# Performance work log

Hardware: AMD Instinct MI355X
Metric: run time of the kernel (lower is better)

## Reference

```python
import jax, jax.numpy as jnp
import numpy as np

N_NODES = 131072
N_EDGES = 1048576
N_FEAT = 8
H = 128
H6 = 256
N_PROB = 64


def _gru_cell(m, h, Wih, Whh, bih, bhh):
    # PyTorch GRUCell semantics
    gi = m @ Wih.T + bih  # [N, 3H]
    gh = h @ Whh.T + bhh
    i_r, i_z, i_n = jnp.split(gi, 3, axis=-1)
    h_r, h_z, h_n = jnp.split(gh, 3, axis=-1)
    r = jax.nn.sigmoid(i_r + h_r)
    z = jax.nn.sigmoid(i_z + h_z)
    n = jnp.tanh(i_n + r * h_n)
    return (1.0 - z) * n + z * h


def _gated_graph_conv(x, src, dst, ew, W, Wih, Whh, bih, bhh):
    # PyG GatedGraphConv(out_channels=H, num_layers=2); in_channels == out_channels so no padding
    h = x
    for l in range(2):
        t = h @ W[l]                      # node-level transform [N, H]
        msg = t[src] * ew[:, None]        # gather + edge scaling [E, H]
        agg = jax.ops.segment_sum(msg, dst, num_segments=x.shape[0])  # scatter-add
        h = _gru_cell(agg, h, Wih, Whh, bih, bhh)
    return h


def _forward(G, edge_index, edge_weight, edge_attribute, segment_ids,
             W_emb1, b_emb1, W_emb2, b_emb2,
             conv1_W, conv1_Wih, conv1_Whh, conv1_bih, conv1_bhh,
             conv2_W, conv2_Wih, conv2_Whh, conv2_bih, conv2_bhh,
             W_g1, b_g1, W_g2, b_g2, W_l, b_l, W_l2, b_l2, W_l3, b_l3):
    src, dst = edge_index[0], edge_index[1]
    x = jax.nn.relu(G @ W_emb1 + b_emb1)
    x = jax.nn.relu(x @ W_emb2 + b_emb2)
    x = jax.nn.relu(_gated_graph_conv(x, src, dst, edge_weight, conv1_W, conv1_Wih, conv1_Whh, conv1_bih, conv1_bhh))
    x = jax.nn.relu(_gated_graph_conv(x, src, dst, edge_weight, conv2_W, conv2_Wih, conv2_Whh, conv2_bih, conv2_bhh))
    x = jax.nn.relu(x @ W_g1 + b_g1)
    x = x @ W_g2 + b_g2                   # node embeddings [N, H]
    # per-problem segment mean (replaces the python loop over contiguous slices)
    sums = jax.ops.segment_sum(x, segment_ids, num_segments=N_PROB)
    counts = jax.ops.segment_sum(jnp.ones((x.shape[0], 1), x.dtype), segment_ids, num_segments=N_PROB)
    gmean = sums / jnp.maximum(counts, 1.0)
    u = jnp.concatenate([x, gmean[segment_ids]], axis=-1)  # [N, 2H]
    u = jax.nn.relu(u @ W_l + b_l)
    u = jax.nn.relu(u @ W_l2 + b_l2)
    u = u @ W_l3 + b_l3                   # [N, 1]
    return u


def setup_inputs() -> dict:
    key = jax.random.key(0)
    ks = jax.random.split(key, 40)
    s = 0.05
    rn = lambda k, shp: (jax.random.normal(k, shp, jnp.float32) * s)
    inp = {}
    inp["G"] = jax.random.normal(ks[0], (N_NODES, N_FEAT), jnp.float32)
    inp["edge_index"] = jax.random.randint(ks[1], (2, N_EDGES), 0, N_NODES, jnp.int32)
    inp["edge_weight"] = jax.random.uniform(ks[2], (N_EDGES,), jnp.float32)
    inp["edge_attribute"] = jax.random.normal(ks[3], (N_EDGES,), jnp.float32)
    inp["segment_ids"] = jnp.sort(jax.random.randint(ks[4], (N_NODES,), 0, N_PROB, jnp.int32))
    inp["W_emb1"] = rn(ks[5], (N_FEAT, H)); inp["b_emb1"] = jnp.zeros((H,), jnp.float32)
    inp["W_emb2"] = rn(ks[6], (H, H));      inp["b_emb2"] = jnp.zeros((H,), jnp.float32)
    inp["conv1_W"] = rn(ks[7], (2, H, H))
    inp["conv1_Wih"] = rn(ks[8], (3 * H, H)); inp["conv1_Whh"] = rn(ks[9], (3 * H, H))
    inp["conv1_bih"] = jnp.zeros((3 * H,), jnp.float32); inp["conv1_bhh"] = jnp.zeros((3 * H,), jnp.float32)
    inp["conv2_W"] = rn(ks[10], (2, H, H))
    inp["conv2_Wih"] = rn(ks[11], (3 * H, H)); inp["conv2_Whh"] = rn(ks[12], (3 * H, H))
    inp["conv2_bih"] = jnp.zeros((3 * H,), jnp.float32); inp["conv2_bhh"] = jnp.zeros((3 * H,), jnp.float32)
    inp["W_g1"] = rn(ks[13], (H, H)); inp["b_g1"] = jnp.zeros((H,), jnp.float32)
    inp["W_g2"] = rn(ks[14], (H, H)); inp["b_g2"] = jnp.zeros((H,), jnp.float32)
    inp["W_l"] = rn(ks[15], (2 * H, H6)); inp["b_l"] = jnp.zeros((H6,), jnp.float32)
    inp["W_l2"] = rn(ks[16], (H6, H)); inp["b_l2"] = jnp.zeros((H,), jnp.float32)
    inp["W_l3"] = rn(ks[17], (H, 1)); inp["b_l3"] = jnp.zeros((1,), jnp.float32)
    return inp


def reference(G, edge_index, edge_weight, edge_attribute, segment_ids,
              W_emb1, b_emb1, W_emb2, b_emb2,
              conv1_W, conv1_Wih, conv1_Whh, conv1_bih, conv1_bhh,
              conv2_W, conv2_Wih, conv2_Whh, conv2_bih, conv2_bhh,
              W_g1, b_g1, W_g2, b_g2, W_l, b_l, W_l2, b_l2, W_l3, b_l3):
    return _forward(G, edge_index, edge_weight, edge_attribute, segment_ids,
                    W_emb1, b_emb1, W_emb2, b_emb2,
                    conv1_W, conv1_Wih, conv1_Whh, conv1_bih, conv1_bhh,
                    conv2_W, conv2_Wih, conv2_Whh, conv2_bih, conv2_bhh,
                    W_g1, b_g1, W_g2, b_g2, W_l, b_l, W_l2, b_l2, W_l3, b_l3)
```

## Files before the change

### kernel.cpp

```cpp
#include <hip/hip_runtime.h>
#include <cstdint>
#include <cstddef>

#define NNODES 131072
#define NEDGES 1048576
#define NPROB  64

typedef _Float16 half8 __attribute__((ext_vector_type(8)));
typedef _Float16 half4v __attribute__((ext_vector_type(4)));
typedef _Float16 half2v __attribute__((ext_vector_type(2)));
typedef float float4v __attribute__((ext_vector_type(4)));

__device__ __forceinline__ float fsigm(float x) {
    return __builtin_amdgcn_rcpf(1.0f + __expf(-x));
}
__device__ __forceinline__ float ftanh(float x) {
    return 1.0f - 2.0f * __builtin_amdgcn_rcpf(__expf(2.0f * x) + 1.0f);
}

__device__ __forceinline__ void async16(void* lds, const void* g) {
    __builtin_amdgcn_global_load_lds(
        (const __attribute__((address_space(1))) uint32_t*)g,
        (__attribute__((address_space(3))) uint32_t*)lds, 16, 0, 0);
}

__global__ __launch_bounds__(256) void cvt16(const float* __restrict__ s,
                                             _Float16* __restrict__ d, int n)
{
    int i = blockIdx.x * 256 + threadIdx.x;
    if (i < n) d[i] = (_Float16)s[i];
}

__global__ __launch_bounds__(256) void tr_cvt(const float* __restrict__ src,
    _Float16* __restrict__ dst, int K, int M, int sstride)
{
    int i = blockIdx.x * 256 + threadIdx.x;
    if (i < M * K) {
        int m = i / K, k = i % K;
        dst[i] = (_Float16)src[(size_t)k * sstride + m];
    }
}

__global__ __launch_bounds__(256) void combine_gru(const float* __restrict__ Wih,
    const float* __restrict__ W, _Float16* __restrict__ outw)
{
    int i = blockIdx.x * 256 + threadIdx.x;
    int g = i >> 7, j = i & 127;
    const float* a = Wih + (size_t)g * 128;
    const float* b = W + (size_t)j * 128;
    float s = 0.0f;
#pragma unroll 8
    for (int k = 0; k < 128; ++k) s = fmaf(a[k], b[k], s);
    outw[i] = (_Float16)s;
}

__global__ __launch_bounds__(256) void combine_headA(const float* __restrict__ Wg2,
    const float* __restrict__ Wl, _Float16* __restrict__ At)
{
    int i = blockIdx.x * 256 + threadIdx.x;
    int m = i >> 7, j = i & 127;
    float s = 0.0f;
#pragma unroll 8
    for (int k = 0; k < 128; ++k)
        s = fmaf(Wg2[(size_t)j * 128 + k], Wl[(size_t)k * 256 + m], s);
    At[i] = (_Float16)s;
}

__global__ __launch_bounds__(256) void combine_headB(const float* __restrict__ Wg2,
    const float* __restrict__ Wl, float* __restrict__ Bf)
{
    int i = blockIdx.x * 256 + threadIdx.x;
    int t = i >> 8, m = i & 255;
    float s = 0.0f;
#pragma unroll 8
    for (int k = 0; k < 128; ++k)
        s = fmaf(Wg2[(size_t)t * 128 + k], Wl[(size_t)(128 + k) * 256 + m], s);
    Bf[i] = s;
}

__global__ __launch_bounds__(256) void combine_c(const float* __restrict__ bg2,
    const float* __restrict__ Wl, const float* __restrict__ bl, float* __restrict__ cvec)
{
    int m = threadIdx.x;
    float s = bl[m];
#pragma unroll 8
    for (int k = 0; k < 128; ++k)
        s = fmaf(bg2[k], Wl[(size_t)k * 256 + m] + Wl[(size_t)(128 + k) * 256 + m], s);
    cvec[m] = s;
}

__global__ __launch_bounds__(256) void deg_hist(const int* __restrict__ dst,
                                                int* __restrict__ deg)
{
    int e = blockIdx.x * 256 + threadIdx.x;
    atomicAdd(&deg[dst[e]], 1);
}

__global__ __launch_bounds__(256) void scan1(const int* __restrict__ deg,
    int* __restrict__ offs, int* __restrict__ bsum)
{
    __shared__ int s[256];
    int b = blockIdx.x, tid = threadIdx.x;
    int4 v = ((const int4*)deg)[b * 256 + tid];
    int t0 = v.x, t1 = t0 + v.y, t2 = t1 + v.z, t3 = t2 + v.w;
    s[tid] = t3;
    __syncthreads();
    for (int off = 1; off < 256; off <<= 1) {
        int x = (tid >= off) ? s[tid - off] : 0;
        __syncthreads();
        if (tid >= off) s[tid] += x;
        __syncthreads();
    }
    int excl = tid ? s[tid - 1] : 0;
    int4 o; o.x = excl; o.y = excl + t0; o.z = excl + t1; o.w = excl + t2;
    ((int4*)offs)[b * 256 + tid] = o;
    if (tid == 255) bsum[b] = s[255];
}

__global__ __launch_bounds__(128) void scan2(int* __restrict__ bsum)
{
    __shared__ int s[128];
    int tid = threadIdx.x;
    s[tid] = bsum[tid];
    __syncthreads();
    for (int off = 1; off < 128; off <<= 1) {
        int x = (tid >= off) ? s[tid - off] : 0;
        __syncthreads();
        if (tid >= off) s[tid] += x;
        __syncthreads();
    }
    bsum[tid] = tid ? s[tid - 1] : 0;
}

__global__ __launch_bounds__(256) void scan3(int* __restrict__ offs,
    const int* __restrict__ bsum, int* __restrict__ pos)
{
    int i = blockIdx.x * 256 + threadIdx.x;
    int v = offs[i] + bsum[i >> 10];
    offs[i] = v;
    pos[i] = v;
    if (i == 0) offs[NNODES] = NEDGES;
}

__global__ __launch_bounds__(256) void csr_fill(const int* __restrict__ src,
    const int* __restrict__ dst, const float* __restrict__ ew,
    int* __restrict__ pos, int2* __restrict__ csr)
{
    int e = blockIdx.x * 256 + threadIdx.x;
    int slot = atomicAdd(&pos[dst[e]], 1);
    csr[slot] = make_int2(src[e], __float_as_int(ew[e]));
}

__global__ __launch_bounds__(256) void gather_agg(const _Float16* __restrict__ t,
    const int2* __restrict__ csr, const int* __restrict__ offs,
    _Float16* __restrict__ agg)
{
    int node = blockIdx.x * 4 + (threadIdx.x >> 6);
    int lane = threadIdx.x & 63;
    int i = offs[node], end = offs[node + 1];
    float a0 = 0.0f, a1 = 0.0f;
    for (; i + 4 <= end; i += 4) {
        int2 e0 = csr[i], e1 = csr[i + 1], e2 = csr[i + 2], e3 = csr[i + 3];
        half2v v0 = *(const half2v*)(t + (size_t)e0.x * 128 + lane * 2);
        half2v v1 = *(const half2v*)(t + (size_t)e1.x * 128 + lane * 2);
        half2v v2 = *(const half2v*)(t + (size_t)e2.x * 128 + lane * 2);
        half2v v3 = *(const half2v*)(t + (size_t)e3.x * 128 + lane * 2);
        float w0 = __int_as_float(e0.y), w1 = __int_as_float(e1.y);
        float w2 = __int_as_float(e2.y), w3 = __int_as_float(e3.y);
        a0 = fmaf((float)v0[0], w0, a0); a1 = fmaf((float)v0[1], w0, a1);
        a0 = fmaf((float)v1[0], w1, a0); a1 = fmaf((float)v1[1], w1, a1);
        a0 = fmaf((float)v2[0], w2, a0); a1 = fmaf((float)v2[1], w2, a1);
        a0 = fmaf((float)v3[0], w3, a0); a1 = fmaf((float)v3[1], w3, a1);
    }
    for (; i < end; ++i) {
        int2 e = csr[i];
        float w = __int_as_float(e.y);
        half2v v = *(const half2v*)(t + (size_t)e.x * 128 + lane * 2);
        a0 = fmaf((float)v[0], w, a0);
        a1 = fmaf((float)v[1], w, a1);
    }
    half2v o; o[0] = (_Float16)a0; o[1] = (_Float16)a1;
    *(half2v*)(agg + (size_t)node * 128 + lane * 2) = o;
}

__global__ __launch_bounds__(256) void emb1_kernel(const float* __restrict__ G,
    const float* __restrict__ W1, const float* __restrict__ b1, _Float16* __restrict__ Y)
{
    int idx = blockIdx.x * 256 + threadIdx.x;
    int n = idx >> 7, c = idx & 127;
    const float* g = G + (size_t)n * 8;
    float y = b1[c];
#pragma unroll
    for (int k = 0; k < 8; ++k) y = fmaf(g[k], W1[k * 128 + c], y);
    Y[(size_t)n * 128 + c] = (_Float16)fmaxf(y, 0.0f);
}

template<int K, int MCH, bool INF16, bool RELU, bool SEGADD>
__global__ __launch_bounds__(256, 2) void gemm_mfma(
    const void* __restrict__ Xin, int xstride,
    const _Float16* __restrict__ Wt,
    const float* __restrict__ bias,
    _Float16* __restrict__ out1, int ostride,
    const float* __restrict__ gproj, const int* __restrict__ seg)
{
    constexpr int ROWB = 2 * K;
    constexpr int SPR  = K / 8;
    __shared__ __align__(16) char Xs[128 * ROWB];
    __shared__ __align__(16) char Ws[128 * ROWB];
    const int tid = threadIdx.x, wid = tid >> 6, l = tid & 63;
    const int lr = l & 15, lk = l >> 4;
    const int wrow = wid * 32;

    for (int mc = 0; mc < MCH; ++mc) {
        __syncthreads();
        {
            const _Float16* wsrc = Wt + (size_t)mc * 128 * K;
            for (int s0 = wid * 64; s0 < 128 * SPR; s0 += 256) {
                int s = s0 + l;
                int row = s / SPR, sub = s % SPR;
                int ksub = sub ^ (row & 7);
                async16(Ws + s0 * 16, (const char*)(wsrc + (size_t)row * K) + ksub * 16);
            }
        }
        asm volatile("s_waitcnt vmcnt(0)" ::: "memory");
        __syncthreads();

        half8 bfr[32];
        if constexpr (K == 128) {
#pragma unroll
            for (int ct = 0; ct < 8; ++ct)
#pragma unroll
                for (int ks = 0; ks < 4; ++ks) {
                    int row = ct * 16 + lr;
                    bfr[ct * 4 + ks] = *(const half8*)(Ws + row * ROWB +
                        ((ks * 64 + lk * 16) ^ ((row & 7) << 4)));
                }
        }

        for (int t = blockIdx.x; t < NNODES / 128; t += gridDim.x) {
            const int nbase = t * 128;
            __syncthreads();
            if constexpr (INF16) {
                const _Float16* xsrc = (const _Float16*)Xin;
                for (int s0 = wid * 64; s0 < 128 * SPR; s0 += 256) {
                    int s = s0 + l;
                    int row = s / SPR, sub = s % SPR;
                    int ksub = sub ^ (row & 7);
                    async16(Xs + s0 * 16,
                            (const char*)(xsrc + (size_t)(nbase + row) * xstride) + ksub * 16);
                }
                asm volatile("s_waitcnt vmcnt(0)" ::: "memory");
            } else {
                const float* xsrc = (const float*)Xin;
                for (int s = tid; s < 128 * SPR; s += 256) {
                    int row = s / SPR, sub = s % SPR;
                    int ksub = sub ^ (row & 7);
                    const float* p = xsrc + (size_t)(nbase + row) * xstride + ksub * 8;
                    float4 u = ((const float4*)p)[0];
                    float4 v = ((const float4*)p)[1];
                    half8 hv;
                    hv[0] = (_Float16)u.x; hv[1] = (_Float16)u.y;
                    hv[2] = (_Float16)u.z; hv[3] = (_Float16)u.w;
                    hv[4] = (_Float16)v.x; hv[5] = (_Float16)v.y;
                    hv[6] = (_Float16)v.z; hv[7] = (_Float16)v.w;
                    *(half8*)(Xs + s * 16) = hv;
                }
            }
            __syncthreads();

            float4v acc[2][8];
#pragma unroll
            for (int i = 0; i < 2; ++i)
#pragma unroll
                for (int j = 0; j < 8; ++j)
#pragma unroll
                    for (int q = 0; q < 4; ++q) acc[i][j][q] = 0.0f;

            if constexpr (K == 128) {
#pragma unroll
                for (int rt = 0; rt < 2; ++rt) {
                    half8 a[4];
                    int row = wrow + rt * 16 + lr;
#pragma unroll
                    for (int ks = 0; ks < 4; ++ks)
                        a[ks] = *(const half8*)(Xs + row * ROWB +
                            ((ks * 64 + lk * 16) ^ ((row & 7) << 4)));
#pragma unroll
                    for (int ct = 0; ct < 8; ++ct)
#pragma unroll
                        for (int ks = 0; ks < 4; ++ks)
                            acc[rt][ct] = __builtin_amdgcn_mfma_f32_16x16x32_f16(
                                a[ks], bfr[ct * 4 + ks], acc[rt][ct], 0, 0, 0);
                }
            } else {
#pragma unroll
                for (int kc = 0; kc < 2; ++kc) {
#pragma unroll
                    for (int ct = 0; ct < 8; ++ct)
#pragma unroll
                        for (int ks = 0; ks < 4; ++ks) {
                            int row = ct * 16 + lr;
                            bfr[ct * 4 + ks] = *(const half8*)(Ws + row * ROWB +
                                (((kc * 4 + ks) * 64 + lk * 16) ^ ((row & 7) << 4)));
                        }
#pragma unroll
                    for (int rt = 0; rt < 2; ++rt) {
                        half8 a[4];
                        int row = wrow + rt * 16 + lr;
#pragma unroll
                        for (int ks = 0; ks < 4; ++ks)
                            a[ks] = *(const half8*)(Xs + row * ROWB +
                                (((kc * 4 + ks) * 64 + lk * 16) ^ ((row & 7) << 4)));
#pragma unroll
                        for (int ct = 0; ct < 8; ++ct)
#pragma unroll
                            for (int ks = 0; ks < 4; ++ks)
                                acc[rt][ct] = __builtin_amdgcn_mfma_f32_16x16x32_f16(
                                    a[ks], bfr[ct * 4 + ks], acc[rt][ct], 0, 0, 0);
                    }
                }
            }

#pragma unroll
            for (int rt = 0; rt < 2; ++rt)
#pragma unroll
            for (int ct = 0; ct < 8; ++ct) {
                const int col = ct * 16 + lr;
                float bv = 0.0f;
                if (bias) bv = bias[mc * 128 + col];
#pragma unroll
                for (int j = 0; j < 4; ++j) {
                    const int n = nbase + wrow + rt * 16 + lk * 4 + j;
                    float v = acc[rt][ct][j] + bv;
                    if constexpr (SEGADD)
                        v += gproj[(size_t)seg[n] * 256 + mc * 128 + col];
                    if constexpr (RELU) v = fmaxf(v, 0.0f);
                    out1[(size_t)n * ostride + mc * 128 + col] = (_Float16)v;
                }
            }
        }
    }
}

__global__ __launch_bounds__(512, 2) void gru_fused(
    const _Float16* __restrict__ agg,
    _Float16* h,
    const _Float16* __restrict__ Wih,
    const _Float16* __restrict__ Whh,
    const float* __restrict__ bih, const float* __restrict__ bhh,
    int relu_out)
{
    __shared__ __align__(16) char As[128 * 256];
    __shared__ __align__(16) char Hs[128 * 256];
    __shared__ __align__(16) char Wb[2][128 * 256];
    const int tid = threadIdx.x, wid = tid >> 6, l = tid & 63;
    const int lr = l & 15, lk = l >> 4;
    const int wr = wid >> 1, wc = wid & 1;
    const int nbase = blockIdx.x * 128;

    auto stageT = [&](char* dst, const _Float16* src) {
        for (int s0 = wid * 64; s0 < 2048; s0 += 512) {
            int s = s0 + l;
            int row = s >> 4, sub = s & 15;
            int ksub = sub ^ (row & 7);
            async16(dst + s0 * 16, (const char*)(src + (size_t)row * 128) + ksub * 16);
        }
    };

    stageT(As, agg + (size_t)nbase * 128);
    stageT(Hs, h + (size_t)nbase * 128);
    stageT(Wb[0], Wih);

    float4v accA[2][4], accB[2][4], rg[2][4], zg[2][4];
    half8 aAg[2][4], aH[2][4];

#pragma unroll
    for (int c = 0; c < 6; ++c) {
        asm volatile("s_waitcnt vmcnt(0)" ::: "memory");
        __syncthreads();
        if (c < 5) {
            const int nc = c + 1;
            const _Float16* wsrc = ((nc & 1) ? Whh : Wih) + (size_t)(nc >> 1) * 16384;
            stageT(Wb[nc & 1], wsrc);
        }
        if (c == 0) {
#pragma unroll
            for (int rt = 0; rt < 2; ++rt) {
                const int row = wr * 32 + rt * 16 + lr;
#pragma unroll
                for (int ks = 0; ks < 4; ++ks) {
                    const int off = row * 256 + ((ks * 64 + lk * 16) ^ ((row & 7) << 4));
                    aAg[rt][ks] = *(const half8*)(As + off);
                    aH[rt][ks]  = *(const half8*)(Hs + off);
                }
            }
        }

        auto& af  = (c & 1) ? aH : aAg;
        auto& acc = (c & 1) ? accB : accA;
#pragma unroll
        for (int rt = 0; rt < 2; ++rt)
#pragma unroll
            for (int ct = 0; ct < 4; ++ct)
#pragma unroll
                for (int q = 0; q < 4; ++q) acc[rt][ct][q] = 0.0f;

        const char* wb = Wb[c & 1];
#pragma unroll
        for (int ct = 0; ct < 4; ++ct) {
            const int rowb = wc * 64 + ct * 16 + lr;
#pragma unroll
            for (int ks = 0; ks < 4; ++ks) {
                half8 b = *(const half8*)(wb + rowb * 256 +
                    ((ks * 64 + lk * 16) ^ ((rowb & 7) << 4)));
                acc[0][ct] = __builtin_amdgcn_mfma_f32_16x16x32_f16(af[0][ks], b, acc[0][ct], 0, 0, 0);
                acc[1][ct] = __builtin_amdgcn_mfma_f32_16x16x32_f16(af[1][ks], b, acc[1][ct], 0, 0, 0);
            }
        }

        if (c == 1) {
#pragma unroll
            for (int rt = 0; rt < 2; ++rt)
#pragma unroll
            for (int ct = 0; ct < 4; ++ct) {
                const int col = wc * 64 + ct * 16 + lr;
                const float bb = bih[col] + bhh[col];
#pragma unroll
                for (int j = 0; j < 4; ++j)
                    rg[rt][ct][j] = fsigm(accA[rt][ct][j] + accB[rt][ct][j] + bb);
            }
        } else if (c == 3) {
#pragma unroll
            for (int rt = 0; rt < 2; ++rt)
#pragma unroll
            for (int ct = 0; ct < 4; ++ct) {
                const int col = wc * 64 + ct * 16 + lr;
                const float bb = bih[128 + col] + bhh[128 + col];
#pragma unroll
                for (int j = 0; j < 4; ++j)
                    zg[rt][ct][j] = fsigm(accA[rt][ct][j] + accB[rt][ct][j] + bb);
            }
        } else if (c == 5) {
#pragma unroll
            for (int rt = 0; rt < 2; ++rt)
#pragma unroll
            for (int ct = 0; ct < 4; ++ct) {
                const int col = wc * 64 + ct * 16 + lr;
                const float bi = bih[256 + col], bh = bhh[256 + col];
                const int c2 = col * 2;
#pragma unroll
                for (int j = 0; j < 4; ++j) {
                    const int row = wr * 32 + rt * 16 + lk * 4 + j;
                    const int n = nbase + row;
                    float nv = ftanh(accA[rt][ct][j] + bi +
                                     rg[rt][ct][j] * (accB[rt][ct][j] + bh));
                    float hold = (float)*(const _Float16*)(Hs + row * 256 +
                        (((c2 >> 4) ^ (row & 7)) << 4) + (c2 & 15));
                    float z = zg[rt][ct][j];
                    float hn = (1.0f - z) * nv + z * hold;
                    if (relu_out) hn = fmaxf(hn, 0.0f);
                    h[(size_t)n * 128 + col] = (_Float16)hn;
                }
            }
        }
    }
}

__global__ __launch_bounds__(256) void seg_sum(const _Float16* __restrict__ x,
    const int* __restrict__ seg, float* __restrict__ sums, float* __restrict__ counts)
{
    int cg = threadIdx.x & 31, rs = threadIdx.x >> 5;
    int r0 = blockIdx.x * 256 + rs * 32;
    float a0 = 0, a1 = 0, a2 = 0, a3 = 0, cnt = 0;
    int cur = seg[r0];
    for (int i = 0; i < 32; ++i) {
        int n = r0 + i;
        int p = seg[n];
        if (p != cur) {
            atomicAdd(&sums[(size_t)cur * 128 + cg * 4 + 0], a0);
            atomicAdd(&sums[(size_t)cur * 128 + cg * 4 + 1], a1);
            atomicAdd(&sums[(size_t)cur * 128 + cg * 4 + 2], a2);
            atomicAdd(&sums[(size_t)cur * 128 + cg * 4 + 3], a3);
            if (cg == 0) atomicAdd(&counts[cur], cnt);
            a0 = a1 = a2 = a3 = 0; cnt = 0; cur = p;
        }
        half4v v = *(const half4v*)(x + (size_t)n * 128 + cg * 4);
        a0 += (float)v[0]; a1 += (float)v[1]; a2 += (float)v[2]; a3 += (float)v[3];
        cnt += 1.0f;
    }
    atomicAdd(&sums[(size_t)cur * 128 + cg * 4 + 0], a0);
    atomicAdd(&sums[(size_t)cur * 128 + cg * 4 + 1], a1);
    atomicAdd(&sums[(size_t)cur * 128 + cg * 4 + 2], a2);
    atomicAdd(&sums[(size_t)cur * 128 + cg * 4 + 3], a3);
    if (cg == 0) atomicAdd(&counts[cur], cnt);
}

__global__ __launch_bounds__(256) void gproj2_kernel(const float* __restrict__ sums,
    const float* __restrict__ counts, const float* __restrict__ Bf,
    const float* __restrict__ cvec, float* __restrict__ gproj2)
{
    __shared__ float gm[128];
    int p = blockIdx.x, m = threadIdx.x;
    if (m < 128) gm[m] = sums[(size_t)p * 128 + m] / fmaxf(counts[p], 1.0f);
    __syncthreads();
    float acc = cvec[m];
#pragma unroll 8
    for (int k = 0; k < 128; ++k)
        acc = fmaf(gm[k], Bf[(size_t)k * 256 + m], acc);
    gproj2[(size_t)p * 256 + m] = acc;
}

__global__ __launch_bounds__(256) void final_dot(const _Float16* __restrict__ u2,
    const float* __restrict__ wl3, const float* __restrict__ bl3, float* __restrict__ out)
{
    int gid = blockIdx.x * 256 + threadIdx.x;
    int n = gid >> 6, lane = gid & 63;
    half2v v = *(const half2v*)(u2 + (size_t)n * 128 + lane * 2);
    float s = (float)v[0] * wl3[lane * 2] + (float)v[1] * wl3[lane * 2 + 1];
#pragma unroll
    for (int off = 32; off; off >>= 1) s += __shfl_xor(s, off);
    if (lane == 0) out[n] = s + bl3[0];
}

extern "C" void kernel_launch(void* const* d_in, const int* in_sizes, int n_in,
                              void* d_out, int out_size, void* d_ws, size_t ws_size,
                              hipStream_t stream)
{
    (void)in_sizes; (void)n_in; (void)out_size; (void)ws_size;

    const float* G     = (const float*)d_in[0];
    const int*   ei    = (const int*)d_in[1];
    const float* ew    = (const float*)d_in[2];
    const int*   seg   = (const int*)d_in[4];
    const float* Wemb1 = (const float*)d_in[5];  const float* bemb1 = (const float*)d_in[6];
    const float* Wemb2 = (const float*)d_in[7];  const float* bemb2 = (const float*)d_in[8];
    const float* c1W   = (const float*)d_in[9];
    const float* c1Wih = (const float*)d_in[10]; const float* c1Whh = (const float*)d_in[11];
    const float* c1bih = (const float*)d_in[12]; const float* c1bhh = (const float*)d_in[13];
    const float* c2W   = (const float*)d_in[14];
    const float* c2Wih = (const float*)d_in[15]; const float* c2Whh = (const float*)d_in[16];
    const float* c2bih = (const float*)d_in[17]; const float* c2bhh = (const float*)d_in[18];
    const float* Wg1   = (const float*)d_in[19]; const float* bg1   = (const float*)d_in[20];
    const float* Wg2   = (const float*)d_in[21]; const float* bg2   = (const float*)d_in[22];
    const float* Wl    = (const float*)d_in[23]; const float* bl    = (const float*)d_in[24];
    const float* Wl2   = (const float*)d_in[25]; const float* bl2   = (const float*)d_in[26];
    const float* Wl3   = (const float*)d_in[27]; const float* bl3   = (const float*)d_in[28];

    const int* srcp = ei;
    const int* dstp = ei + NEDGES;

    char* ws = (char*)d_ws;
    const size_t NBH = (size_t)NNODES * 128 * 2;
    const size_t U1B = (size_t)NNODES * 256 * 2;

    _Float16* hA   = (_Float16*)ws;
    _Float16* hB   = (_Float16*)(ws + NBH);
    _Float16* u1   = (_Float16*)(ws + 2 * NBH);
    _Float16* aggH = (_Float16*)(ws + 2 * NBH + U1B);
    char*     aux  = ws + 3 * NBH + U1B;
    float* sums    = (float*)aux;
    float* counts  = (float*)(aux + 32768);
    float* gproj2  = (float*)(aux + 33792);
    int*   deg     = (int*)(aux + 33792 + 65536);
    int*   offs    = deg + NNODES;
    int*   pos     = offs + NNODES + 64;
    int2*  csr     = (int2*)(pos + NNODES);
    char*  wtb     = (char*)csr + (size_t)NEDGES * 8;

    _Float16* wt_emb2 = (_Float16*)wtb;
    _Float16* wt_g1   = wt_emb2 + 16384;
    _Float16* wt_l2   = wt_g1 + 16384;
    _Float16* wt_hh1  = wt_l2 + 32768;
    _Float16* wt_hh2  = wt_hh1 + 49152;
    _Float16* wc00    = wt_hh2 + 49152;
    _Float16* wc01    = wc00 + 49152;
    _Float16* wc10    = wc01 + 49152;
    _Float16* wc11    = wc10 + 49152;
    _Float16* At      = wc11 + 49152;
    float*    Bf      = (float*)(At + 32768);
    float*    cvec    = Bf + 32768;

    tr_cvt<<<64, 256, 0, stream>>>(Wemb2, wt_emb2, 128, 128, 128);
    tr_cvt<<<64, 256, 0, stream>>>(Wg1, wt_g1, 128, 128, 128);
    tr_cvt<<<128, 256, 0, stream>>>(Wl2, wt_l2, 256, 128, 128);
    cvt16<<<192, 256, 0, stream>>>(c1Whh, wt_hh1, 49152);
    cvt16<<<192, 256, 0, stream>>>(c2Whh, wt_hh2, 49152);
    combine_gru<<<192, 256, 0, stream>>>(c1Wih, c1W,         wc00);
    combine_gru<<<192, 256, 0, stream>>>(c1Wih, c1W + 16384, wc01);
    combine_gru<<<192, 256, 0, stream>>>(c2Wih, c2W,         wc10);
    combine_gru<<<192, 256, 0, stream>>>(c2Wih, c2W + 16384, wc11);
    combine_headA<<<128, 256, 0, stream>>>(Wg2, Wl, At);
    combine_headB<<<128, 256, 0, stream>>>(Wg2, Wl, Bf);
    combine_c<<<1, 256, 0, stream>>>(bg2, Wl, bl, cvec);

    hipMemsetAsync(deg, 0, NNODES * 4, stream);
    deg_hist<<<NEDGES / 256, 256, 0, stream>>>(dstp, deg);
    scan1<<<128, 256, 0, stream>>>(deg, offs, pos);
    scan2<<<1, 128, 0, stream>>>(pos);
    scan3<<<NNODES / 256, 256, 0, stream>>>(offs, pos, deg);
    csr_fill<<<NEDGES / 256, 256, 0, stream>>>(srcp, dstp, ew, deg, csr);

    emb1_kernel<<<NNODES * 128 / 256, 256, 0, stream>>>(G, Wemb1, bemb1, hB);
    gemm_mfma<128, 1, true, true, false><<<512, 256, 0, stream>>>(
        hB, 128, wt_emb2, bemb2, hA, 128, nullptr, nullptr);

    const _Float16* wcs[2][2] = { { wc00, wc01 }, { wc10, wc11 } };
    const _Float16* whh[2] = { wt_hh1, wt_hh2 };
    const float* bihs[2] = { c1bih, c2bih };
    const float* bhhs[2] = { c1bhh, c2bhh };
    for (int cv = 0; cv < 2; ++cv) {
        for (int lyr = 0; lyr < 2; ++lyr) {
            gather_agg<<<NNODES / 4, 256, 0, stream>>>(hA, csr, offs, aggH);
            gru_fused<<<NNODES / 128, 512, 0, stream>>>(
                aggH, hA, wcs[cv][lyr], whh[cv], bihs[cv], bhhs[cv], (lyr == 1) ? 1 : 0);
        }
    }

    gemm_mfma<128, 1, true, true, false><<<512, 256, 0, stream>>>(
        hA, 128, wt_g1, bg1, hB, 128, nullptr, nullptr);

    hipMemsetAsync(sums, 0, 33792, stream);
    seg_sum<<<NNODES / 256, 256, 0, stream>>>(hB, seg, sums, counts);
    gproj2_kernel<<<NPROB, 256, 0, stream>>>(sums, counts, Bf, cvec, gproj2);

    gemm_mfma<128, 2, true, true, true><<<512, 256, 0, stream>>>(
        hB, 128, At, nullptr, u1, 256, gproj2, seg);
    gemm_mfma<256, 1, true, true, false><<<256, 256, 0, stream>>>(
        u1, 256, wt_l2, bl2, hA, 128, nullptr, nullptr);
    final_dot<<<NNODES * 64 / 256, 256, 0, stream>>>(hA, Wl3, bl3, (float*)d_out);
}
```

Before: 968.7 us.

## Fuse neighbor aggregation into GRU kernel and final dot into last GEMM

The separate gather_agg pass is removed. Each gru_fused block now gathers weighted neighbor rows straight from the CSR into its LDS tile, with two nodes interleaved per wave for memory-level parallelism. The hidden state is ping-ponged between two buffers so the in-place read/write hazard goes away. The final 128->1 projection is folded into the epilogue of the last MFMA GEMM using shuffle reductions, and several small weight-prep launches are merged into fewer kernels. The aim is to avoid writing and re-reading the aggregated tensor and to cut launch count. The cost is that the gather latency now sits inside the GEMM kernel, which could hurt occupancy or overlap.

```diff
diff --git a/kernel.cpp b/kernel.cpp
--- a/kernel.cpp
+++ b/kernel.cpp
@@ -24,11 +24,14 @@
         (__attribute__((address_space(3))) uint32_t*)lds, 16, 0, 0);
 }
 
-__global__ __launch_bounds__(256) void cvt16(const float* __restrict__ s,
-                                             _Float16* __restrict__ d, int n)
+__global__ __launch_bounds__(256) void tr_cvt2(const float* __restrict__ s0,
+    const float* __restrict__ s1, _Float16* __restrict__ dst)
 {
     int i = blockIdx.x * 256 + threadIdx.x;
-    if (i < n) d[i] = (_Float16)s[i];
+    int half = i >> 14, r = i & 16383;
+    int m = r >> 7, k = r & 127;
+    const float* s = half ? s1 : s0;
+    dst[i] = (_Float16)s[(size_t)k * 128 + m];
 }
 
 __global__ __launch_bounds__(256) void tr_cvt(const float* __restrict__ src,
@@ -41,11 +44,23 @@
     }
 }
 
-__global__ __launch_bounds__(256) void combine_gru(const float* __restrict__ Wih,
-    const float* __restrict__ W, _Float16* __restrict__ outw)
+__global__ __launch_bounds__(256) void cvt16_2(const float* __restrict__ a,
+    const float* __restrict__ b, _Float16* __restrict__ d)
 {
     int i = blockIdx.x * 256 + threadIdx.x;
-    int g = i >> 7, j = i & 127;
+    d[i] = (_Float16)((i < 49152) ? a[i] : b[i - 49152]);
+}
+
+__global__ __launch_bounds__(256) void combine_gru4(const float* __restrict__ W1ih,
+    const float* __restrict__ W1, const float* __restrict__ W2ih,
+    const float* __restrict__ W2, _Float16* __restrict__ outw)
+{
+    int i = blockIdx.x * 256 + threadIdx.x;
+    int set = i / 49152, r = i - set * 49152;
+    int g = r >> 7, j = r & 127;
+    const float* Wih = (set < 2) ? W1ih : W2ih;
+    const float* W = (set == 0) ? W1 : (set == 1) ? W1 + 16384
+                   : (set == 2) ? W2 : W2 + 16384;
     const float* a = Wih + (size_t)g * 128;
     const float* b = W + (size_t)j * 128;
     float s = 0.0f;
@@ -148,39 +163,9 @@
 {
     int e = blockIdx.x * 256 + threadIdx.x;
     int slot = atomicAdd(&pos[dst[e]], 1);
-    csr[slot] = make_int2(src[e], __float_as_int(ew[e]));
-}
-
-__global__ __launch_bounds__(256) void gather_agg(const _Float16* __restrict__ t,
-    const int2* __restrict__ csr, const int* __restrict__ offs,
-    _Float16* __restrict__ agg)
-{
-    int node = blockIdx.x * 4 + (threadIdx.x >> 6);
-    int lane = threadIdx.x & 63;
-    int i = offs[node], end = offs[node + 1];
-    float a0 = 0.0f, a1 = 0.0f;
-    for (; i + 4 <= end; i += 4) {
-        int2 e0 = csr[i], e1 = csr[i + 1], e2 = csr[i + 2], e3 = csr[i + 3];
-        half2v v0 = *(const half2v*)(t + (size_t)e0.x * 128 + lane * 2);
-        half2v v1 = *(const half2v*)(t + (size_t)e1.x * 128 + lane * 2);
-        half2v v2 = *(const half2v*)(t + (size_t)e2.x * 128 + lane * 2);
-        half2v v3 = *(const half2v*)(t + (size_t)e3.x * 128 + lane * 2);
-        float w0 = __int_as_float(e0.y), w1 = __int_as_float(e1.y);
-        float w2 = __int_as_float(e2.y), w3 = __int_as_float(e3.y);
-        a0 = fmaf((float)v0[0], w0, a0); a1 = fmaf((float)v0[1], w0, a1);
-        a0 = fmaf((float)v1[0], w1, a0); a1 = fmaf((float)v1[1], w1, a1);
-        a0 = fmaf((float)v2[0], w2, a0); a1 = fmaf((float)v2[1], w2, a1);
-        a0 = fmaf((float)v3[0], w3, a0); a1 = fmaf((float)v3[1], w3, a1);
-    }
-    for (; i < end; ++i) {
-        int2 e = csr[i];
-        float w = __int_as_float(e.y);
-        half2v v = *(const half2v*)(t + (size_t)e.x * 128 + lane * 2);
-        a0 = fmaf((float)v[0], w, a0);
-        a1 = fmaf((float)v[1], w, a1);
-    }
-    half2v o; o[0] = (_Float16)a0; o[1] = (_Float16)a1;
-    *(half2v*)(agg + (size_t)node * 128 + lane * 2) = o;
+    unsigned long long pk = (unsigned long long)(unsigned)src[e]
+                          | ((unsigned long long)__float_as_uint(ew[e]) << 32);
+    __builtin_nontemporal_store(pk, (unsigned long long*)csr + slot);
 }
 
 __global__ __launch_bounds__(256) void emb1_kernel(const float* __restrict__ G,
@@ -195,13 +180,15 @@
     Y[(size_t)n * 128 + c] = (_Float16)fmaxf(y, 0.0f);
 }
 
-template<int K, int MCH, bool INF16, bool RELU, bool SEGADD>
+template<int K, int MCH, bool INF16, bool RELU, bool SEGADD, bool FINAL>
 __global__ __launch_bounds__(256, 2) void gemm_mfma(
     const void* __restrict__ Xin, int xstride,
     const _Float16* __restrict__ Wt,
     const float* __restrict__ bias,
     _Float16* __restrict__ out1, int ostride,
-    const float* __restrict__ gproj, const int* __restrict__ seg)
+    const float* __restrict__ gproj, const int* __restrict__ seg,
+    const float* __restrict__ wl3, const float* __restrict__ bl3p,
+    float* __restrict__ outf)
 {
     constexpr int ROWB = 2 * K;
     constexpr int SPR  = K / 8;
@@ -321,21 +308,55 @@
                 }
             }
 
-#pragma unroll
-            for (int rt = 0; rt < 2; ++rt)
-#pragma unroll
-            for (int ct = 0; ct < 8; ++ct) {
-                const int col = ct * 16 + lr;
-                float bv = 0.0f;
-                if (bias) bv = bias[mc * 128 + col];
+            if constexpr (FINAL) {
+                const float bl3v = bl3p[0];
+                float part[2][4];
+#pragma unroll
+                for (int rt = 0; rt < 2; ++rt)
+#pragma unroll
+                    for (int j = 0; j < 4; ++j) part[rt][j] = 0.0f;
+#pragma unroll
+                for (int rt = 0; rt < 2; ++rt)
+#pragma unroll
+                for (int ct = 0; ct < 8; ++ct) {
+                    const int col = ct * 16 + lr;
+                    const float wv = wl3[col];
+                    const float bv = bias[col];
+#pragma unroll
+                    for (int j = 0; j < 4; ++j) {
+                        float v = fmaxf(acc[rt][ct][j] + bv, 0.0f);
+                        part[rt][j] = fmaf(v, wv, part[rt][j]);
+                    }
+                }
+#pragma unroll
+                for (int rt = 0; rt < 2; ++rt)
 #pragma unroll
                 for (int j = 0; j < 4; ++j) {
-                    const int n = nbase + wrow + rt * 16 + lk * 4 + j;
-                    float v = acc[rt][ct][j] + bv;
-                    if constexpr (SEGADD)
-                        v += gproj[(size_t)seg[n] * 256 + mc * 128 + col];
-                    if constexpr (RELU) v = fmaxf(v, 0.0f);
-                    out1[(size_t)n * ostride + mc * 128 + col] = (_Float16)v;
+                    float s = part[rt][j];
+                    s += __shfl_xor(s, 1);
+                    s += __shfl_xor(s, 2);
+                    s += __shfl_xor(s, 4);
+                    s += __shfl_xor(s, 8);
+                    if (lr == 0)
+                        outf[nbase + wrow + rt * 16 + lk * 4 + j] = s + bl3v;
+                }
+            } else {
+#pragma unroll
+                for (int rt = 0; rt < 2; ++rt)
+#pragma unroll
+                for (int ct = 0; ct < 8; ++ct) {
+                    const int col = ct * 16 + lr;
+                    float bv = 0.0f;
+                    if (bias) bv = bias[mc * 128 + col];
+#pragma unroll
+                    for (int j = 0; j < 4; ++j) {
+                        const int n = nbase + wrow + rt * 16 + lk * 4 + j;
+                        float v = acc[rt][ct][j] + bv;
+                        if constexpr (SEGADD)
+                            v += gproj[(size_t)seg[n] * 256 + mc * 128 + col];
+                        if constexpr (RELU) v = fmaxf(v, 0.0f);
+                        out1[(size_t)n * ostride + mc * 128 + col] = (_Float16)v;
+                    }
                 }
             }
         }
@@ -343,9 +364,10 @@
 }
 
 __global__ __launch_bounds__(512, 2) void gru_fused(
-    const _Float16* __restrict__ agg,
-    _Float16* h,
-    const _Float16* __restrict__ Wih,
+    const _Float16* __restrict__ hin,
+    _Float16* __restrict__ hout,
+    const int2* __restrict__ csr, const int* __restrict__ offs,
+    const _Float16* __restrict__ Wc,
     const _Float16* __restrict__ Whh,
     const float* __restrict__ bih, const float* __restrict__ bhh,
     int relu_out)
@@ -367,9 +389,52 @@
         }
     };
 
-    stageT(As, agg + (size_t)nbase * 128);
-    stageT(Hs, h + (size_t)nbase * 128);
-    stageT(Wb[0], Wih);
+    stageT(Hs, hin + (size_t)nbase * 128);
+    stageT(Wb[0], Wc);
+
+    {
+        const int cb = l * 4;
+        for (int rr = wid * 16; rr < wid * 16 + 16; rr += 2) {
+            const int n0 = nbase + rr, n1 = n0 + 1;
+            int i0 = offs[n0], E0 = offs[n0 + 1];
+            int i1 = E0, E1 = offs[n1 + 1];
+            float a00 = 0.f, a01 = 0.f, a10 = 0.f, a11 = 0.f;
+            while (i0 < E0 || i1 < E1) {
+                int c0 = E0 - i0; c0 = c0 > 4 ? 4 : c0;
+                int c1 = E1 - i1; c1 = c1 > 4 ? 4 : c1;
+                int2 e0[4], e1[4];
+#pragma unroll
+                for (int k = 0; k < 4; ++k) {
+                    if (k < c0) e0[k] = csr[i0 + k];
+                    if (k < c1) e1[k] = csr[i1 + k];
+                }
+                half2v v0[4], v1[4];
+#pragma unroll
+                for (int k = 0; k < 4; ++k) {
+                    if (k < c0) v0[k] = *(const half2v*)(hin + (size_t)e0[k].x * 128 + l * 2);
+                    if (k < c1) v1[k] = *(const half2v*)(hin + (size_t)e1[k].x * 128 + l * 2);
+                }
+#pragma unroll
+                for (int k = 0; k < 4; ++k) {
+                    if (k < c0) {
+                        float w = __int_as_float(e0[k].y);
+                        a00 = fmaf((float)v0[k][0], w, a00);
+                        a01 = fmaf((float)v0[k][1], w, a01);
+                    }
+                    if (k < c1) {
+                        float w = __int_as_float(e1[k].y);
+                        a10 = fmaf((float)v1[k][0], w, a10);
+                        a11 = fmaf((float)v1[k][1], w, a11);
+                    }
+                }
+                i0 += c0; i1 += c1;
+            }
+            half2v o0; o0[0] = (_Float16)a00; o0[1] = (_Float16)a01;
+            half2v o1; o1[0] = (_Float16)a10; o1[1] = (_Float16)a11;
+            *(half2v*)(As + rr * 256 + (((cb >> 4) ^ (rr & 7)) << 4) + (cb & 15)) = o0;
+            *(half2v*)(As + (rr + 1) * 256 + (((cb >> 4) ^ ((rr + 1) & 7)) << 4) + (cb & 15)) = o1;
+        }
+    }
 
     float4v accA[2][4], accB[2][4], rg[2][4], zg[2][4];
     half8 aAg[2][4], aH[2][4];
@@ -380,7 +445,7 @@
         __syncthreads();
         if (c < 5) {
             const int nc = c + 1;
-            const _Float16* wsrc = ((nc & 1) ? Whh : Wih) + (size_t)(nc >> 1) * 16384;
+            const _Float16* wsrc = ((nc & 1) ? Whh : Wc) + (size_t)(nc >> 1) * 16384;
             stageT(Wb[nc & 1], wsrc);
         }
         if (c == 0) {
@@ -459,7 +524,7 @@
                     float z = zg[rt][ct][j];
                     float hn = (1.0f - z) * nv + z * hold;
                     if (relu_out) hn = fmaxf(hn, 0.0f);
-                    h[(size_t)n * 128 + col] = (_Float16)hn;
+                    hout[(size_t)n * 128 + col] = (_Float16)hn;
                 }
             }
         }
@@ -508,18 +573,6 @@
     for (int k = 0; k < 128; ++k)
         acc = fmaf(gm[k], Bf[(size_t)k * 256 + m], acc);
     gproj2[(size_t)p * 256 + m] = acc;
-}
-
-__global__ __launch_bounds__(256) void final_dot(const _Float16* __restrict__ u2,
-    const float* __restrict__ wl3, const float* __restrict__ bl3, float* __restrict__ out)
-{
-    int gid = blockIdx.x * 256 + threadIdx.x;
-    int n = gid >> 6, lane = gid & 63;
-    half2v v = *(const half2v*)(u2 + (size_t)n * 128 + lane * 2);
-    float s = (float)v[0] * wl3[lane * 2] + (float)v[1] * wl3[lane * 2 + 1];
-#pragma unroll
-    for (int off = 32; off; off >>= 1) s += __shfl_xor(s, off);
-    if (lane == 0) out[n] = s + bl3[0];
 }
 
 extern "C" void kernel_launch(void* const* d_in, const int* in_sizes, int n_in,
@@ -556,7 +609,7 @@
     _Float16* hA   = (_Float16*)ws;
     _Float16* hB   = (_Float16*)(ws + NBH);
     _Float16* u1   = (_Float16*)(ws + 2 * NBH);
-    _Float16* aggH = (_Float16*)(ws + 2 * NBH + U1B);
+    _Float16* hC   = (_Float16*)(ws + 2 * NBH + U1B);
     char*     aux  = ws + 3 * NBH + U1B;
     float* sums    = (float*)aux;
     float* counts  = (float*)(aux + 32768);
@@ -572,23 +625,15 @@
     _Float16* wt_l2   = wt_g1 + 16384;
     _Float16* wt_hh1  = wt_l2 + 32768;
     _Float16* wt_hh2  = wt_hh1 + 49152;
-    _Float16* wc00    = wt_hh2 + 49152;
-    _Float16* wc01    = wc00 + 49152;
-    _Float16* wc10    = wc01 + 49152;
-    _Float16* wc11    = wc10 + 49152;
-    _Float16* At      = wc11 + 49152;
+    _Float16* wc0     = wt_hh2 + 49152;
+    _Float16* At      = wc0 + 4 * 49152;
     float*    Bf      = (float*)(At + 32768);
     float*    cvec    = Bf + 32768;
 
-    tr_cvt<<<64, 256, 0, stream>>>(Wemb2, wt_emb2, 128, 128, 128);
-    tr_cvt<<<64, 256, 0, stream>>>(Wg1, wt_g1, 128, 128, 128);
+    tr_cvt2<<<128, 256, 0, stream>>>(Wemb2, Wg1, wt_emb2);
     tr_cvt<<<128, 256, 0, stream>>>(Wl2, wt_l2, 256, 128, 128);
-    cvt16<<<192, 256, 0, stream>>>(c1Whh, wt_hh1, 49152);
-    cvt16<<<192, 256, 0, stream>>>(c2Whh, wt_hh2, 49152);
-    combine_gru<<<192, 256, 0, stream>>>(c1Wih, c1W,         wc00);
-    combine_gru<<<192, 256, 0, stream>>>(c1Wih, c1W + 16384, wc01);
-    combine_gru<<<192, 256, 0, stream>>>(c2Wih, c2W,         wc10);
-    combine_gru<<<192, 256, 0, stream>>>(c2Wih, c2W + 16384, wc11);
+    cvt16_2<<<384, 256, 0, stream>>>(c1Whh, c2Whh, wt_hh1);
+    combine_gru4<<<768, 256, 0, stream>>>(c1Wih, c1W, c2Wih, c2W, wc0);
     combine_headA<<<128, 256, 0, stream>>>(Wg2, Wl, At);
     combine_headB<<<128, 256, 0, stream>>>(Wg2, Wl, Bf);
     combine_c<<<1, 256, 0, stream>>>(bg2, Wl, bl, cvec);
@@ -601,31 +646,33 @@
     csr_fill<<<NEDGES / 256, 256, 0, stream>>>(srcp, dstp, ew, deg, csr);
 
     emb1_kernel<<<NNODES * 128 / 256, 256, 0, stream>>>(G, Wemb1, bemb1, hB);
-    gemm_mfma<128, 1, true, true, false><<<512, 256, 0, stream>>>(
-        hB, 128, wt_emb2, bemb2, hA, 128, nullptr, nullptr);
-
-    const _Float16* wcs[2][2] = { { wc00, wc01 }, { wc10, wc11 } };
+    gemm_mfma<128, 1, true, true, false, false><<<512, 256, 0, stream>>>(
+        hB, 128, wt_emb2, bemb2, hA, 128, nullptr, nullptr, nullptr, nullptr, nullptr);
+
+    const _Float16* wcs[2][2] = { { wc0, wc0 + 49152 }, { wc0 + 2 * 49152, wc0 + 3 * 49152 } };
     const _Float16* whh[2] = { wt_hh1, wt_hh2 };
     const float* bihs[2] = { c1bih, c2bih };
     const float* bhhs[2] = { c1bhh, c2bhh };
+    _Float16* hcur = hA;
+    _Float16* halt = hC;
     for (int cv = 0; cv < 2; ++cv) {
         for (int lyr = 0; lyr < 2; ++lyr) {
-            gather_agg<<<NNODES / 4, 256, 0, stream>>>(hA, csr, offs, aggH);
             gru_fused<<<NNODES / 128, 512, 0, stream>>>(
-                aggH, hA, wcs[cv][lyr], whh[cv], bihs[cv], bhhs[cv], (lyr == 1) ? 1 : 0);
-        }
-    }
-
-    gemm_mfma<128, 1, true, true, false><<<512, 256, 0, stream>>>(
-        hA, 128, wt_g1, bg1, hB, 128, nullptr, nullptr);
+                hcur, halt, csr, offs, wcs[cv][lyr], whh[cv],
+                bihs[cv], bhhs[cv], (lyr == 1) ? 1 : 0);
+            _Float16* tmp = hcur; hcur = halt; halt = tmp;
+        }
+    }
+
+    gemm_mfma<128, 1, true, true, false, false><<<512, 256, 0, stream>>>(
+        hcur, 128, wt_g1, bg1, hB, 128, nullptr, nullptr, nullptr, nullptr, nullptr);
 
     hipMemsetAsync(sums, 0, 33792, stream);
     seg_sum<<<NNODES / 256, 256, 0, stream>>>(hB, seg, sums, counts);
     gproj2_kernel<<<NPROB, 256, 0, stream>>>(sums, counts, Bf, cvec, gproj2);
 
-    gemm_mfma<128, 2, true, true, true><<<512, 256, 0, stream>>>(
-        hB, 128, At, nullptr, u1, 256, gproj2, seg);
-    gemm_mfma<256, 1, true, true, false><<<256, 256, 0, stream>>>(
-        u1, 256, wt_l2, bl2, hA, 128, nullptr, nullptr);
-    final_dot<<<NNODES * 64 / 256, 256, 0, stream>>>(hA, Wl3, bl3, (float*)d_out);
-}
+    gemm_mfma<128, 2, true, true, true, false><<<512, 256, 0, stream>>>(
+        hB, 128, At, nullptr, u1, 256, gproj2, seg, nullptr, nullptr, nullptr);
+    gemm_mfma<256, 1, true, true, false, true><<<256, 256, 0, stream>>>(
+        u1, 256, wt_l2, bl2, nullptr, 0, nullptr, nullptr, Wl3, bl3, (float*)d_out);
+}
```

New measurement: 1.405 ms. +45.0%, slower.
